# Kernel optimization log

Measured on AMD Instinct MI355X. Metric: run time of the kernel, lower is better.

Reference implementation:

```python
import jax, jax.numpy as jnp
import numpy as np

B, N, D, K, L, H, DFF = 2048, 64, 256, 32, 2, 8, 1024
TEMP = 10.0
EPS = 1e-10


def _ln(x, g, b):
    m = jnp.mean(x, -1, keepdims=True)
    v = jnp.mean((x - m) ** 2, -1, keepdims=True)
    return (x - m) * jax.lax.rsqrt(v + 1e-5) * g + b


def _mha(x, Wqkv, bqkv, Wo, bo):
    b, n, d = x.shape
    dh = d // H
    qkv = x @ Wqkv.T + bqkv                      # [b,n,3d]
    q, k, v = jnp.split(qkv, 3, axis=-1)
    q = q.reshape(b, n, H, dh)
    k = k.reshape(b, n, H, dh)
    v = v.reshape(b, n, H, dh)
    att = jnp.einsum('bqhd,bkhd->bhqk', q, k) / np.float32(np.sqrt(dh))
    att = jax.nn.softmax(att, axis=-1)
    o = jnp.einsum('bhqk,bkhd->bqhd', att, v).reshape(b, n, d)
    return o @ Wo.T + bo


def _encoder(x, Wqkv, bqkv, Wo, bo, ln1_g, ln1_b, ln2_g, ln2_b, W1, b1, W2, b2):
    # torch TransformerEncoder, norm_first=False (post-LN), dropout=0
    for l in range(L):
        x = _ln(x + _mha(x, Wqkv[l], bqkv[l], Wo[l], bo[l]), ln1_g[l], ln1_b[l])
        h = jax.nn.relu(x @ W1[l].T + b1[l]) @ W2[l].T + b2[l]
        x = _ln(x + h, ln2_g[l], ln2_b[l])
    return x


def _cluster_probs_from_emb(emb, mus):
    # ||x - tanh(mu)||^2 via expansion to avoid the [B,N,K,D] intermediate
    mt = jnp.tanh(mus)                                       # [K,D]
    d2 = (jnp.sum(emb ** 2, -1)[..., None]
          - 2.0 * jnp.einsum('bnd,kd->bnk', emb, mt)
          + jnp.sum(mt ** 2, -1))                            # [B,N,K]
    e = jnp.exp(-d2 / TEMP)
    return e / jnp.sum(e, -1, keepdims=True)


def _forward(input_series, init_logits, transition_logits,
             Wqkv, bqkv, Wo, bo, ln1_g, ln1_b, ln2_g, ln2_b,
             W1, b1, W2, b2, mus):
    prob_pi = jax.nn.softmax(init_logits, axis=0)            # [K]
    prob_A = jax.nn.softmax(transition_logits, axis=1)       # [K,K]
    emb_all = _encoder(input_series, Wqkv, bqkv, Wo, bo,
                       ln1_g, ln1_b, ln2_g, ln2_b, W1, b1, W2, b2)
    logits_all = _cluster_probs_from_emb(emb_all, mus)       # [B,N,K]

    log_emit = jnp.log(logits_all + EPS)                     # [B,N,K]
    lt0 = jax.nn.softmax(jnp.log(prob_pi + EPS)[None, :] + log_emit[:, 0], axis=1)

    def step(lt, le):
        lt = jax.nn.softmax(jnp.log(lt @ prob_A + EPS) + le, axis=1)
        return lt, lt

    _, rest = jax.lax.scan(step, lt0, jnp.swapaxes(log_emit[:, 1:], 0, 1))
    cluster_probs = jnp.concatenate([lt0[:, None], jnp.swapaxes(rest, 0, 1)], axis=1)
    entropy_loss = -jnp.mean(jnp.sum(cluster_probs * jnp.log(cluster_probs + EPS), -1))
    return cluster_probs, emb_all, prob_pi, prob_A, entropy_loss


def setup_inputs() -> dict:
    key = jax.random.key(0)
    ks = jax.random.split(key, 10)
    s = jnp.float32(0.02)
    return {
        'input_series': jax.random.normal(ks[0], (B, N, D), jnp.float32),
        'init_logits': jax.random.normal(ks[1], (K,), jnp.float32),
        'transition_logits': jax.random.normal(ks[2], (K, K), jnp.float32),
        'Wqkv': jax.random.normal(ks[3], (L, 3 * D, D), jnp.float32) * s,
        'bqkv': jnp.zeros((L, 3 * D), jnp.float32),
        'Wo': jax.random.normal(ks[4], (L, D, D), jnp.float32) * s,
        'bo': jnp.zeros((L, D), jnp.float32),
        'ln1_g': jnp.ones((L, D), jnp.float32),
        'ln1_b': jnp.zeros((L, D), jnp.float32),
        'ln2_g': jnp.ones((L, D), jnp.float32),
        'ln2_b': jnp.zeros((L, D), jnp.float32),
        'W1': jax.random.normal(ks[5], (L, DFF, D), jnp.float32) * s,
        'b1': jnp.zeros((L, DFF), jnp.float32),
        'W2': jax.random.normal(ks[6], (L, D, DFF), jnp.float32) * s,
        'b2': jnp.zeros((L, D), jnp.float32),
        'mus': jax.random.normal(ks[7], (K, D), jnp.float32),
    }


def reference(input_series, init_logits, transition_logits, Wqkv, bqkv, Wo, bo,
              ln1_g, ln1_b, ln2_g, ln2_b, W1, b1, W2, b2, mus):
    return _forward(input_series, init_logits, transition_logits, Wqkv, bqkv,
                    Wo, bo, ln1_g, ln1_b, ln2_g, ln2_b, W1, b1, W2, b2, mus)
```

## Files before the change

kernel.cpp:

```cpp
#include <hip/hip_runtime.h>

#define BB   2048
#define NNX  64
#define DD   256
#define KKC  32
#define LLN  2
#define HHN  8
#define DHH  32
#define DFFN 1024
#define BNT  (BB*NNX)

typedef short s16x8 __attribute__((ext_vector_type(8)));
typedef float f32x4 __attribute__((ext_vector_type(4)));

#define GLOAD_LDS16(gp, lp) __builtin_amdgcn_global_load_lds( \
    (const __attribute__((address_space(1))) void*)(gp),      \
    (__attribute__((address_space(3))) void*)(lp), 16, 0, 0)

#define WAITVM4() asm volatile("s_waitcnt vmcnt(4)" ::: "memory")
#define WAITVM0() asm volatile("s_waitcnt vmcnt(0)" ::: "memory")
#define WAITLGKM0() do { asm volatile("s_waitcnt lgkmcnt(0)" ::: "memory"); \
                         __builtin_amdgcn_sched_barrier(0); } while (0)
#define SBAR() __builtin_amdgcn_s_barrier()

__device__ __forceinline__ unsigned short f2bf(float f) {
  unsigned int u = __float_as_uint(f);
  u += 0x7fffu + ((u >> 16) & 1u);
  return (unsigned short)(u >> 16);
}
__device__ __forceinline__ float bf2f(unsigned short u) {
  return __uint_as_float(((unsigned int)u) << 16);
}

__global__ __launch_bounds__(256) void cvt_kernel(const float4* __restrict__ src,
                                                  ushort4* __restrict__ dst, int n4) {
  int i = blockIdx.x * 256 + threadIdx.x;
  int st = gridDim.x * 256;
  for (; i < n4; i += st) {
    float4 v = src[i];
    ushort4 o;
    o.x = f2bf(v.x); o.y = f2bf(v.y); o.z = f2bf(v.z); o.w = f2bf(v.w);
    dst[i] = o;
  }
}

__global__ __launch_bounds__(256) void cvtw_kernel(const float4* __restrict__ wq, ushort4* __restrict__ dq,
                                                   const float4* __restrict__ wo, ushort4* __restrict__ dov,
                                                   const float4* __restrict__ w1, ushort4* __restrict__ d1,
                                                   const float4* __restrict__ w2, ushort4* __restrict__ d2) {
  const int n0 = 98304, n1 = 32768, n2 = 131072, n3 = 131072;
  int i = blockIdx.x * 256 + threadIdx.x;
  int st = gridDim.x * 256;
  for (; i < n0 + n1 + n2 + n3; i += st) {
    const float4* s; ushort4* d; int j = i;
    if (j < n0) { s = wq; d = dq; }
    else if ((j -= n0) < n1) { s = wo; d = dov; }
    else if ((j -= n1) < n2) { s = w1; d = d1; }
    else { j -= n2; s = w2; d = d2; }
    float4 v = s[j];
    ushort4 o;
    o.x = f2bf(v.x); o.y = f2bf(v.y); o.z = f2bf(v.z); o.w = f2bf(v.w);
    d[j] = o;
  }
}

__global__ void mt_kernel(const float* __restrict__ mus, unsigned short* __restrict__ mtb,
                          float* __restrict__ mtn) {
  int k = threadIdx.x;
  if (k < 32) {
    float acc = 0.f;
    for (int d = 0; d < 256; d++) {
      float t = tanhf(mus[k * 256 + d]);
      mtb[k * 264 + d] = f2bf(t);
      acc += t * t;
    }
    mtn[k] = acc;
  }
}

__global__ void piA_kernel(const float* __restrict__ il, const float* __restrict__ tl,
                           float* __restrict__ d_pi, float* __restrict__ d_A,
                           float* __restrict__ d_ent) {
  int lane = threadIdx.x;
  if (lane == 0) *d_ent = 0.f;
  if (lane < 32) {
    float v = il[lane];
    float mx = v;
    #pragma unroll
    for (int off = 16; off; off >>= 1) mx = fmaxf(mx, __shfl_xor(mx, off, 32));
    float e = expf(v - mx), sm = e;
    #pragma unroll
    for (int off = 16; off; off >>= 1) sm += __shfl_xor(sm, off, 32);
    d_pi[lane] = e / sm;
    for (int r = 0; r < 32; r++) {
      float a = tl[r * 32 + lane];
      float m2 = a;
      #pragma unroll
      for (int off = 16; off; off >>= 1) m2 = fmaxf(m2, __shfl_xor(m2, off, 32));
      float e2 = expf(a - m2), s2 = e2;
      #pragma unroll
      for (int off = 16; off; off >>= 1) s2 += __shfl_xor(s2, off, 32);
      d_A[r * 32 + lane] = e2 / s2;
    }
  }
}

template <int EPI>
__global__ __launch_bounds__(256, 4) void gemm_nt(const unsigned short* __restrict__ A,
                                                  const unsigned short* __restrict__ Bw,
                                                  const float* __restrict__ bias,
                                                  unsigned short* __restrict__ outp,
                                                  int N, int K, int nx) {
  __shared__ unsigned short lds[16384];
  const int t = threadIdx.x;
  const int bid = blockIdx.x, nwg = gridDim.x;
  const int wg = (bid & 7) * (nwg >> 3) + (bid >> 3);
  const int m0 = (wg / nx) << 7;
  const int n0 = (wg % nx) << 7;
  const int lane = t & 63, w = t >> 6;
  const int wm = w >> 1, wn = w & 1;
  const int lr = lane & 15, lk = lane >> 4;

  const int r0 = t >> 2, sg = t & 3;
  const int s0 = sg ^ ((r0 >> 1) & 3);
  const int r1 = r0 + 64;
  const int s1 = sg ^ ((r1 >> 1) & 3);
  const int aoff0 = (m0 + r0) * K + s0 * 8;
  const int aoff1 = (m0 + r1) * K + s1 * 8;
  const int boff0 = (n0 + r0) * K + s0 * 8;
  const int boff1 = (n0 + r1) * K + s1 * 8;

#define STAGE(buf, k0) do {                                    \
    char* la = (char*)lds + (buf) * 16384;                     \
    GLOAD_LDS16(A + aoff0 + (k0), la + t * 16);                \
    GLOAD_LDS16(A + aoff1 + (k0), la + 4096 + t * 16);         \
    GLOAD_LDS16(Bw + boff0 + (k0), la + 8192 + t * 16);        \
    GLOAD_LDS16(Bw + boff1 + (k0), la + 12288 + t * 16);       \
  } while (0)

  f32x4 acc[4][4];
  #pragma unroll
  for (int i = 0; i < 4; i++)
    #pragma unroll
    for (int j = 0; j < 4; j++) acc[i][j] = (f32x4)(0.f);

  const int ra = wm * 64 + lr, rb = wn * 64 + lr;
  const int sla = lk ^ ((ra >> 1) & 3), slb = lk ^ ((rb >> 1) & 3);

  const int NT = K >> 5;
  STAGE(0, 0);
  STAGE(1, 32);
  WAITVM4();
  SBAR();

  int c = 0;
  for (int kt = 0; kt < NT; kt++) {
    s16x8 af[4], bf[4];
    {
      const unsigned short* ua = lds + c * 8192;
      const unsigned short* ub = ua + 4096;
      #pragma unroll
      for (int mf = 0; mf < 4; mf++)
        af[mf] = *(const s16x8*)&ua[(ra + mf * 16) * 32 + sla * 8];
      #pragma unroll
      for (int nf = 0; nf < 4; nf++)
        bf[nf] = *(const s16x8*)&ub[(rb + nf * 16) * 32 + slb * 8];
    }
    __builtin_amdgcn_s_setprio(1);
    #pragma unroll
    for (int mf = 0; mf < 4; mf++)
      #pragma unroll
      for (int nf = 0; nf < 4; nf++)
        acc[mf][nf] = __builtin_amdgcn_mfma_f32_16x16x32_bf16(af[mf], bf[nf], acc[mf][nf], 0, 0, 0);
    __builtin_amdgcn_s_setprio(0);
    SBAR();
    if (kt < NT - 2) {
      STAGE(c, (kt + 2) << 5);
      WAITVM4();
    } else if (kt == NT - 2) {
      WAITVM0();
    }
    SBAR();
    c ^= 1;
  }
#undef STAGE

  #pragma unroll
  for (int nf = 0; nf < 4; nf++) {
    int col = n0 + wn * 64 + nf * 16 + lr;
    float bv = bias[col];
    #pragma unroll
    for (int mf = 0; mf < 4; mf++)
      #pragma unroll
      for (int r = 0; r < 4; r++) {
        int row = m0 + wm * 64 + mf * 16 + lk * 4 + r;
        float v = acc[mf][nf][r] + bv;
        if (EPI == 1) v = fmaxf(v, 0.f);
        outp[(size_t)row * N + col] = f2bf(v);
      }
  }
}

template <bool WR32>
__global__ __launch_bounds__(512) void gemm_ln(const unsigned short* __restrict__ A,
                                               const unsigned short* __restrict__ Bw,
                                               const float* __restrict__ bias,
                                               const unsigned short* __restrict__ res,
                                               const float* __restrict__ g,
                                               const float* __restrict__ bta,
                                               unsigned short* __restrict__ xb,
                                               float* __restrict__ x32,
                                               int K) {
  __shared__ unsigned short As[128 * 64];
  __shared__ unsigned short Bs[256 * 64];
  __shared__ float stats[2][128][4];
  const int t = threadIdx.x;
  const int nwg = gridDim.x;
  const int bid = blockIdx.x;
  const int wg = (bid & 7) * (nwg >> 3) + (bid >> 3);
  const int m0 = wg << 7;

  const int lane = t & 63, w = t >> 6;
  const int wm = w >> 2, wn = w & 3;
  const int lr = lane & 15, lk = lane >> 4;

  size_t aoff[2], boff[4];
  #pragma unroll
  for (int p = 0; p < 2; p++) {
    int u = p * 512 + t;
    int row = u >> 3, sp = u & 7;
    int seg = sp ^ (((row >> 2) & 1) << 1);
    aoff[p] = (size_t)(m0 + row) * K + seg * 8;
  }
  #pragma unroll
  for (int p = 0; p < 4; p++) {
    int u = p * 512 + t;
    int row = u >> 3, sp = u & 7;
    int seg = sp ^ (((row >> 2) & 1) << 1);
    boff[p] = (size_t)row * K + seg * 8;
  }

  f32x4 acc[4][4];
  #pragma unroll
  for (int i = 0; i < 4; i++)
    #pragma unroll
    for (int j = 0; j < 4; j++) acc[i][j] = (f32x4)(0.f);

  for (int k0 = 0; k0 < K; k0 += 64) {
    #pragma unroll
    for (int p = 0; p < 2; p++)
      GLOAD_LDS16(A + aoff[p] + k0, (char*)As + (p * 512 + t) * 16);
    #pragma unroll
    for (int p = 0; p < 4; p++)
      GLOAD_LDS16(Bw + boff[p] + k0, (char*)Bs + (p * 512 + t) * 16);
    __syncthreads();
    #pragma unroll
    for (int z = 0; z < 2; z++) {
      s16x8 af[4], bfr[4];
      #pragma unroll
      for (int mf = 0; mf < 4; mf++) {
        int row = wm * 64 + mf * 16 + lr;
        int cc = (z * 4 + lk) ^ (((row >> 2) & 1) << 1);
        af[mf] = *(const s16x8*)&As[row * 64 + cc * 8];
      }
      #pragma unroll
      for (int nf = 0; nf < 4; nf++) {
        int row = wn * 64 + nf * 16 + lr;
        int cc = (z * 4 + lk) ^ (((row >> 2) & 1) << 1);
        bfr[nf] = *(const s16x8*)&Bs[row * 64 + cc * 8];
      }
      #pragma unroll
      for (int mf = 0; mf < 4; mf++)
        #pragma unroll
        for (int nf = 0; nf < 4; nf++)
          acc[mf][nf] = __builtin_amdgcn_mfma_f32_16x16x32_bf16(af[mf], bfr[nf], acc[mf][nf], 0, 0, 0);
    }
    __syncthreads();
  }

  float bv[4];
  #pragma unroll
  for (int nf = 0; nf < 4; nf++) bv[nf] = bias[wn * 64 + nf * 16 + lr];

  #pragma unroll
  for (int mf = 0; mf < 4; mf++) {
    #pragma unroll
    for (int r = 0; r < 4; r++) {
      int grow = m0 + wm * 64 + mf * 16 + lk * 4 + r;
      float s = 0.f, q = 0.f;
      #pragma unroll
      for (int nf = 0; nf < 4; nf++) {
        int col = wn * 64 + nf * 16 + lr;
        float v = acc[mf][nf][r] + bv[nf] + bf2f(res[(size_t)grow * 256 + col]);
        acc[mf][nf][r] = v;
        s += v; q += v * v;
      }
      #pragma unroll
      for (int off = 1; off < 16; off <<= 1) { s += __shfl_xor(s, off); q += __shfl_xor(q, off); }
      if (lr == 0) {
        int lrow = wm * 64 + mf * 16 + lk * 4 + r;
        stats[0][lrow][wn] = s;
        stats[1][lrow][wn] = q;
      }
    }
  }
  __syncthreads();

  float gv[4], bbv[4];
  #pragma unroll
  for (int nf = 0; nf < 4; nf++) {
    int col = wn * 64 + nf * 16 + lr;
    gv[nf] = g[col]; bbv[nf] = bta[col];
  }
  #pragma unroll
  for (int mf = 0; mf < 4; mf++) {
    #pragma unroll
    for (int r = 0; r < 4; r++) {
      int lrow = wm * 64 + mf * 16 + lk * 4 + r;
      int grow = m0 + lrow;
      float s4 = stats[0][lrow][0] + stats[0][lrow][1] + stats[0][lrow][2] + stats[0][lrow][3];
      float q4 = stats[1][lrow][0] + stats[1][lrow][1] + stats[1][lrow][2] + stats[1][lrow][3];
      float mean = s4 * (1.f / 256.f);
      float var = q4 * (1.f / 256.f) - mean * mean;
      float rs = rsqrtf(var + 1e-5f);
      #pragma unroll
      for (int nf = 0; nf < 4; nf++) {
        int col = wn * 64 + nf * 16 + lr;
        float val = (acc[mf][nf][r] - mean) * rs * gv[nf] + bbv[nf];
        xb[(size_t)grow * 256 + col] = f2bf(val);
        if (WR32) x32[(size_t)grow * 256 + col] = val;
      }
    }
  }
}

__global__ __launch_bounds__(64) void attn_kernel(const unsigned short* __restrict__ qkv,
                                                  unsigned short* __restrict__ ob) {
  __shared__ unsigned short al[6784];
  unsigned short* qs = al;
  unsigned short* ks = al + 2048;
  unsigned short* vs = al + 4608;
  unsigned short* vt = al;
  unsigned short* ps = al + 2176;
  const int bh = blockIdx.x;
  const int b = bh >> 3, h = bh & 7;
  const int lane = threadIdx.x;
  const int lr = lane & 15, lk = lane >> 4;

  #pragma unroll
  for (int p = 0; p < 4; p++) {
    int u = lane + p * 64;
    int row = u >> 2, seg = u & 3;
    size_t gb = (size_t)(b * 64 + row) * 768 + h * 32 + seg * 8;
    GLOAD_LDS16(qkv + gb, (char*)al + u * 16);
    GLOAD_LDS16(qkv + gb + 256, (char*)al + 4096 + u * 16);
    GLOAD_LDS16(qkv + gb + 512, (char*)al + 9216 + u * 16);
  }
  __syncthreads();

  s16x8 aq[4], bk[4], vchunk[4];
  #pragma unroll
  for (int mi = 0; mi < 4; mi++) aq[mi] = *(const s16x8*)&qs[(mi * 16 + lr) * 32 + lk * 8];
  #pragma unroll
  for (int nj = 0; nj < 4; nj++) bk[nj] = *(const s16x8*)&ks[(nj * 16 + lr) * 32 + lk * 8];
  const int vrow = lane >> 2, vcs = (lane & 3) * 8;
  #pragma unroll
  for (int q = 0; q < 4; q++)
    vchunk[q] = *(const s16x8*)&vs[(q * 16 + vrow) * 32 + vcs];
  WAITLGKM0();

  #pragma unroll
  for (int q = 0; q < 4; q++)
    #pragma unroll
    for (int j = 0; j < 8; j++)
      vt[(vcs + j) * 68 + q * 16 + vrow] = (unsigned short)vchunk[q][j];

  f32x4 s[4][4];
  #pragma unroll
  for (int i = 0; i < 4; i++)
    #pragma unroll
    for (int j = 0; j < 4; j++) s[i][j] = (f32x4)(0.f);
  #pragma unroll
  for (int mi = 0; mi < 4; mi++)
    #pragma unroll
    for (int nj = 0; nj < 4; nj++)
      s[mi][nj] = __builtin_amdgcn_mfma_f32_16x16x32_bf16(aq[mi], bk[nj], s[mi][nj], 0, 0, 0);

  const float scale = 0.17677669529663687f;
  #pragma unroll
  for (int mi = 0; mi < 4; mi++) {
    #pragma unroll
    for (int r = 0; r < 4; r++) {
      float t0 = s[mi][0][r] * scale, t1 = s[mi][1][r] * scale;
      float t2 = s[mi][2][r] * scale, t3 = s[mi][3][r] * scale;
      float mx = fmaxf(fmaxf(t0, t1), fmaxf(t2, t3));
      #pragma unroll
      for (int off = 8; off; off >>= 1) mx = fmaxf(mx, __shfl_xor(mx, off, 16));
      float e0 = expf(t0 - mx), e1 = expf(t1 - mx), e2 = expf(t2 - mx), e3 = expf(t3 - mx);
      float sm = e0 + e1 + e2 + e3;
      #pragma unroll
      for (int off = 8; off; off >>= 1) sm += __shfl_xor(sm, off, 16);
      float inv = 1.f / sm;
      int prow = mi * 16 + lk * 4 + r;
      ps[prow * 72 + lr + 0]  = f2bf(e0 * inv);
      ps[prow * 72 + lr + 16] = f2bf(e1 * inv);
      ps[prow * 72 + lr + 32] = f2bf(e2 * inv);
      ps[prow * 72 + lr + 48] = f2bf(e3 * inv);
    }
  }
  WAITLGKM0();

  f32x4 oacc[4][2];
  #pragma unroll
  for (int i = 0; i < 4; i++) { oacc[i][0] = (f32x4)(0.f); oacc[i][1] = (f32x4)(0.f); }
  #pragma unroll
  for (int kk = 0; kk < 2; kk++) {
    s16x8 bv[2];
    #pragma unroll
    for (int nf = 0; nf < 2; nf++)
      bv[nf] = *(const s16x8*)&vt[(nf * 16 + lr) * 68 + kk * 32 + lk * 8];
    #pragma unroll
    for (int mi = 0; mi < 4; mi++) {
      s16x8 ap = *(const s16x8*)&ps[(mi * 16 + lr) * 72 + kk * 32 + lk * 8];
      #pragma unroll
      for (int nf = 0; nf < 2; nf++)
        oacc[mi][nf] = __builtin_amdgcn_mfma_f32_16x16x32_bf16(ap, bv[nf], oacc[mi][nf], 0, 0, 0);
    }
  }
  #pragma unroll
  for (int mi = 0; mi < 4; mi++)
    #pragma unroll
    for (int nf = 0; nf < 2; nf++)
      #pragma unroll
      for (int r = 0; r < 4; r++) {
        int tok = mi * 16 + lk * 4 + r;
        int c = nf * 16 + lr;
        ob[(size_t)(b * 64 + tok) * 256 + h * 32 + c] = f2bf(oacc[mi][nf][r]);
      }
}

__global__ __launch_bounds__(256) void cluster_kernel(const unsigned short* __restrict__ xb,
                                                      const unsigned short* __restrict__ mtb,
                                                      const float* __restrict__ mtn,
                                                      float* __restrict__ log_emit) {
  __shared__ unsigned short ms[32 * 264];
  const int t = threadIdx.x;
  for (int i = t; i < 2112; i += 256)
    ((uint2*)ms)[i] = ((const uint2*)mtb)[i];
  const int lane = t & 63, w = t >> 6;
  const int lr = lane & 15, lk = lane >> 4;
  const float mtn0 = mtn[lr], mtn1 = mtn[16 + lr];
  __syncthreads();

  const size_t tok0 = (size_t)blockIdx.x * 256 + (size_t)w * 64;
  f32x4 s[4][2];
  #pragma unroll
  for (int i = 0; i < 4; i++) { s[i][0] = (f32x4)(0.f); s[i][1] = (f32x4)(0.f); }

  #pragma unroll
  for (int kk = 0; kk < 8; kk++) {
    s16x8 bf0 = *(const s16x8*)&ms[lr * 264 + lk * 8 + kk * 32];
    s16x8 bf1 = *(const s16x8*)&ms[(16 + lr) * 264 + lk * 8 + kk * 32];
    #pragma unroll
    for (int mi = 0; mi < 4; mi++) {
      s16x8 af = *(const s16x8*)&xb[(tok0 + mi * 16 + lr) * 256 + lk * 8 + kk * 32];
      s[mi][0] = __builtin_amdgcn_mfma_f32_16x16x32_bf16(af, bf0, s[mi][0], 0, 0, 0);
      s[mi][1] = __builtin_amdgcn_mfma_f32_16x16x32_bf16(af, bf1, s[mi][1], 0, 0, 0);
    }
  }

  #pragma unroll
  for (int mi = 0; mi < 4; mi++) {
    #pragma unroll
    for (int r = 0; r < 4; r++) {
      float l0 = (2.f * s[mi][0][r] - mtn0) * 0.1f;
      float l1 = (2.f * s[mi][1][r] - mtn1) * 0.1f;
      float mx = fmaxf(l0, l1);
      #pragma unroll
      for (int off = 8; off; off >>= 1) mx = fmaxf(mx, __shfl_xor(mx, off, 16));
      float e0 = expf(l0 - mx), e1 = expf(l1 - mx);
      float sm = e0 + e1;
      #pragma unroll
      for (int off = 8; off; off >>= 1) sm += __shfl_xor(sm, off, 16);
      float inv = 1.f / sm;
      size_t row = tok0 + mi * 16 + lk * 4 + r;
      log_emit[row * 32 + lr]      = logf(e0 * inv + 1e-10f);
      log_emit[row * 32 + 16 + lr] = logf(e1 * inv + 1e-10f);
    }
  }
}

__global__ __launch_bounds__(256) void scan_kernel(const float* __restrict__ log_emit,
                                                   const float* __restrict__ pi,
                                                   const float* __restrict__ A,
                                                   float* __restrict__ cp,
                                                   float* __restrict__ ent) {
  const int g = threadIdx.x >> 5, j = threadIdx.x & 31;
  const int batch = blockIdx.x * 8 + g;
  float regA[32];
  #pragma unroll
  for (int i = 0; i < 32; i++) regA[i] = A[i * 32 + j];
  const float* le = log_emit + (size_t)batch * 64 * 32;
  float* cpo = cp + (size_t)batch * 64 * 32;

  float u = logf(pi[j] + 1e-10f) + le[j];
  float mx = u;
  #pragma unroll
  for (int off = 16; off; off >>= 1) mx = fmaxf(mx, __shfl_xor(mx, off, 32));
  float e = expf(u - mx), sm = e;
  #pragma unroll
  for (int off = 16; off; off >>= 1) sm += __shfl_xor(sm, off, 32);
  float p = e / sm;
  cpo[j] = p;
  float enta = p * logf(p + 1e-10f);

  for (int n = 1; n < 64; n++) {
    float tt = 0.f;
    #pragma unroll
    for (int i = 0; i < 32; i++) tt += __shfl(p, i, 32) * regA[i];
    u = logf(tt + 1e-10f) + le[n * 32 + j];
    mx = u;
    #pragma unroll
    for (int off = 16; off; off >>= 1) mx = fmaxf(mx, __shfl_xor(mx, off, 32));
    e = expf(u - mx); sm = e;
    #pragma unroll
    for (int off = 16; off; off >>= 1) sm += __shfl_xor(sm, off, 32);
    p = e / sm;
    cpo[n * 32 + j] = p;
    enta += p * logf(p + 1e-10f);
  }
  #pragma unroll
  for (int off = 16; off; off >>= 1) enta += __shfl_xor(enta, off, 32);
  if (j == 0) atomicAdd(ent, -enta * (1.f / (2048.f * 64.f)));
}

extern "C" void kernel_launch(void* const* d_in, const int* in_sizes, int n_in,
                              void* d_out, int out_size, void* d_ws, size_t ws_size,
                              hipStream_t stream) {
  const float* input = (const float*)d_in[0];
  const float* init_logits = (const float*)d_in[1];
  const float* trans = (const float*)d_in[2];
  const float* Wqkv = (const float*)d_in[3];
  const float* bqkv = (const float*)d_in[4];
  const float* Wo = (const float*)d_in[5];
  const float* bo = (const float*)d_in[6];
  const float* ln1g = (const float*)d_in[7];
  const float* ln1b = (const float*)d_in[8];
  const float* ln2g = (const float*)d_in[9];
  const float* ln2b = (const float*)d_in[10];
  const float* W1 = (const float*)d_in[11];
  const float* b1 = (const float*)d_in[12];
  const float* W2 = (const float*)d_in[13];
  const float* b2 = (const float*)d_in[14];
  const float* mus = (const float*)d_in[15];

  float* out = (float*)d_out;
  float* cp = out;
  float* x = out + 4194304;
  float* d_pi = out + 37748736;
  float* d_A = out + 37748768;
  float* d_ent = out + 37749792;

  char* ws = (char*)d_ws;
  unsigned short* qkv = (unsigned short*)ws;
  unsigned short* hb = (unsigned short*)ws;
  float* log_emit = (float*)ws;
  unsigned short* ob = (unsigned short*)(ws + 268435456ull);
  unsigned short* xb = (unsigned short*)(ws + 335544320ull);
  unsigned short* wq_b = (unsigned short*)(ws + 402653184ull);
  unsigned short* wo_b = (unsigned short*)(ws + 402653184ull + 786432ull);
  unsigned short* w1_b = (unsigned short*)(ws + 402653184ull + 1048576ull);
  unsigned short* w2_b = (unsigned short*)(ws + 402653184ull + 2097152ull);
  unsigned short* mtb = (unsigned short*)(ws + 402653184ull + 3145728ull);
  float* mtn = (float*)(ws + 402653184ull + 3178496ull);

  cvt_kernel<<<2048, 256, 0, stream>>>((const float4*)input, (ushort4*)xb, BNT * 256 / 4);
  cvtw_kernel<<<512, 256, 0, stream>>>((const float4*)Wqkv, (ushort4*)wq_b,
                                       (const float4*)Wo, (ushort4*)wo_b,
                                       (const float4*)W1, (ushort4*)w1_b,
                                       (const float4*)W2, (ushort4*)w2_b);
  mt_kernel<<<1, 64, 0, stream>>>(mus, mtb, mtn);
  piA_kernel<<<1, 64, 0, stream>>>(init_logits, trans, d_pi, d_A, d_ent);

  for (int l = 0; l < 2; l++) {
    gemm_nt<0><<<6144, 256, 0, stream>>>(xb, wq_b + l * 196608, bqkv + l * 768,
                                         qkv, 768, 256, 6);
    attn_kernel<<<16384, 64, 0, stream>>>(qkv, ob);
    gemm_ln<false><<<1024, 512, 0, stream>>>(ob, wo_b + l * 65536, bo + l * 256,
                                             xb, ln1g + l * 256, ln1b + l * 256,
                                             xb, nullptr, 256);
    gemm_nt<1><<<8192, 256, 0, stream>>>(xb, w1_b + l * 262144, b1 + l * 1024,
                                         hb, 1024, 256, 8);
    if (l == LLN - 1)
      gemm_ln<true><<<1024, 512, 0, stream>>>(hb, w2_b + l * 262144, b2 + l * 256,
                                              xb, ln2g + l * 256, ln2b + l * 256,
                                              xb, x, 1024);
    else
      gemm_ln<false><<<1024, 512, 0, stream>>>(hb, w2_b + l * 262144, b2 + l * 256,
                                               xb, ln2g + l * 256, ln2b + l * 256,
                                               xb, nullptr, 1024);
  }

  cluster_kernel<<<512, 256, 0, stream>>>(xb, mtb, mtn, log_emit);
  scan_kernel<<<256, 256, 0, stream>>>(log_emit, d_pi, d_A, cp, d_ent);
}
```

Before: 1.141 ms.

## Split FFN2 GEMM+LayerNorm into tiled gemm_nt with residual plus separate LN kernel

Replaces the fused gemm_ln kernel for the second FFN projection (K=1024) with the generic 128x128-tile gemm_nt, extended with a residual-add epilogue that writes a bf16 pre-norm buffer, followed by a standalone per-token LayerNorm kernel. The goal is to use the better-pipelined gemm_nt main loop (double-buffered global_load_lds) for the long-K GEMM instead of the 128x256 full-row tile that gemm_ln needs for fused LN, which runs with fewer blocks. In exchange it adds an extra round trip through HBM for the intermediate activations and rounds the pre-LN sum to bf16.

```diff
diff --git a/kernel.cpp b/kernel.cpp
--- a/kernel.cpp
+++ b/kernel.cpp
@@ -109,6 +109,7 @@
 __global__ __launch_bounds__(256, 4) void gemm_nt(const unsigned short* __restrict__ A,
                                                   const unsigned short* __restrict__ Bw,
                                                   const float* __restrict__ bias,
+                                                  const unsigned short* __restrict__ res,
                                                   unsigned short* __restrict__ outp,
                                                   int N, int K, int nx) {
   __shared__ unsigned short lds[16384];
@@ -194,9 +195,11 @@
       #pragma unroll
       for (int r = 0; r < 4; r++) {
         int row = m0 + wm * 64 + mf * 16 + lk * 4 + r;
+        size_t o = (size_t)row * N + col;
         float v = acc[mf][nf][r] + bv;
         if (EPI == 1) v = fmaxf(v, 0.f);
-        outp[(size_t)row * N + col] = f2bf(v);
+        if (EPI == 2) v += bf2f(res[o]);
+        outp[o] = f2bf(v);
       }
   }
 }
@@ -331,6 +334,36 @@
         if (WR32) x32[(size_t)grow * 256 + col] = val;
       }
     }
+  }
+}
+
+template <bool WR32>
+__global__ __launch_bounds__(256) void ln_kernel(const unsigned short* __restrict__ yin,
+                                                 const float* __restrict__ g,
+                                                 const float* __restrict__ bta,
+                                                 unsigned short* __restrict__ xb,
+                                                 float* __restrict__ xout) {
+  const int w = threadIdx.x >> 6, lane = threadIdx.x & 63;
+  const size_t tok = (size_t)blockIdx.x * 4 + w;
+  ushort4 u = *((const ushort4*)(yin + tok * 256) + lane);
+  float v[4] = {bf2f(u.x), bf2f(u.y), bf2f(u.z), bf2f(u.w)};
+  float s = v[0] + v[1] + v[2] + v[3];
+  float q = v[0] * v[0] + v[1] * v[1] + v[2] * v[2] + v[3] * v[3];
+  #pragma unroll
+  for (int off = 1; off < 64; off <<= 1) { s += __shfl_xor(s, off); q += __shfl_xor(q, off); }
+  float mean = s * (1.f / 256.f);
+  float var = q * (1.f / 256.f) - mean * mean;
+  float rs = rsqrtf(var + 1e-5f);
+  int d0 = lane * 4;
+  float o0 = (v[0] - mean) * rs * g[d0 + 0] + bta[d0 + 0];
+  float o1 = (v[1] - mean) * rs * g[d0 + 1] + bta[d0 + 1];
+  float o2 = (v[2] - mean) * rs * g[d0 + 2] + bta[d0 + 2];
+  float o3 = (v[3] - mean) * rs * g[d0 + 3] + bta[d0 + 3];
+  ushort4 ub = {f2bf(o0), f2bf(o1), f2bf(o2), f2bf(o3)};
+  *((ushort4*)(xb + tok * 256) + lane) = ub;
+  if (WR32) {
+    float4 fo = {o0, o1, o2, o3};
+    *((float4*)(xout + tok * 256) + lane) = fo;
   }
 }
 
@@ -566,6 +599,7 @@
   unsigned short* hb = (unsigned short*)ws;
   float* log_emit = (float*)ws;
   unsigned short* ob = (unsigned short*)(ws + 268435456ull);
+  unsigned short* y2 = ob;
   unsigned short* xb = (unsigned short*)(ws + 335544320ull);
   unsigned short* wq_b = (unsigned short*)(ws + 402653184ull);
   unsigned short* wo_b = (unsigned short*)(ws + 402653184ull + 786432ull);
@@ -584,21 +618,19 @@
 
   for (int l = 0; l < 2; l++) {
     gemm_nt<0><<<6144, 256, 0, stream>>>(xb, wq_b + l * 196608, bqkv + l * 768,
-                                         qkv, 768, 256, 6);
+                                         nullptr, qkv, 768, 256, 6);
     attn_kernel<<<16384, 64, 0, stream>>>(qkv, ob);
     gemm_ln<false><<<1024, 512, 0, stream>>>(ob, wo_b + l * 65536, bo + l * 256,
                                              xb, ln1g + l * 256, ln1b + l * 256,
                                              xb, nullptr, 256);
     gemm_nt<1><<<8192, 256, 0, stream>>>(xb, w1_b + l * 262144, b1 + l * 1024,
-                                         hb, 1024, 256, 8);
+                                         nullptr, hb, 1024, 256, 8);
+    gemm_nt<2><<<2048, 256, 0, stream>>>(hb, w2_b + l * 262144, b2 + l * 256,
+                                         xb, y2, 256, 1024, 2);
     if (l == LLN - 1)
-      gemm_ln<true><<<1024, 512, 0, stream>>>(hb, w2_b + l * 262144, b2 + l * 256,
-                                              xb, ln2g + l * 256, ln2b + l * 256,
-                                              xb, x, 1024);
+      ln_kernel<true><<<32768, 256, 0, stream>>>(y2, ln2g + l * 256, ln2b + l * 256, xb, x);
     else
-      gemm_ln<false><<<1024, 512, 0, stream>>>(hb, w2_b + l * 262144, b2 + l * 256,
-                                               xb, ln2g + l * 256, ln2b + l * 256,
-                                               xb, nullptr, 1024);
+      ln_kernel<false><<<32768, 256, 0, stream>>>(y2, ln2g + l * 256, ln2b + l * 256, xb, nullptr);
   }
 
   cluster_kernel<<<512, 256, 0, stream>>>(xb, mtb, mtn, log_emit);
```

Result: slower. 1.290 ms (+13.0%).

## Quantize FFN hidden activations and W2 to FP8 and run second FFN GEMM in FP8

Applied to the files above, without the earlier changes.

The FFN1 epilogue now writes the ReLU output as scaled FP8 (e4m3) instead of bf16, and W2 is converted to scaled FP8. A new gemm_ln_fp8 kernel uses FP8 MFMA with the residual-add and LayerNorm fused in, undoing the scales in the epilogue. This halves the traffic for the large hidden tensor and doubles MFMA throughput for the W2 GEMM. It costs accuracy through FP8 rounding and fixed scale factors, and the new kernel uses a simple unpipelined single-buffer loop.

```diff
diff --git a/kernel.cpp b/kernel.cpp
--- a/kernel.cpp
+++ b/kernel.cpp
@@ -32,6 +32,24 @@
   return __uint_as_float(((unsigned int)u) << 16);
 }
 
+__device__ __forceinline__ unsigned char f2fp8(float f) {
+  unsigned u = __float_as_uint(f);
+  unsigned lsb = (u >> 20) & 1u;
+  u += 0x7FFFFu + lsb;
+  int e = (int)((u >> 23) & 255u) - 120;
+  if (e <= 0) {
+    int q = (int)(f * 512.f + 0.5f);
+    return (unsigned char)q;
+  }
+  if (e > 15) return 0x7E;
+  return (unsigned char)((e << 3) | ((u >> 20) & 7u));
+}
+__device__ __forceinline__ unsigned char f2fp8s(float f) {
+  unsigned s = __float_as_uint(f) >> 31;
+  float a = fminf(fabsf(f), 448.f);
+  return (unsigned char)((s << 7) | f2fp8(a));
+}
+
 __global__ __launch_bounds__(256) void cvt_kernel(const float4* __restrict__ src,
                                                   ushort4* __restrict__ dst, int n4) {
   int i = blockIdx.x * 256 + threadIdx.x;
@@ -47,20 +65,27 @@
 __global__ __launch_bounds__(256) void cvtw_kernel(const float4* __restrict__ wq, ushort4* __restrict__ dq,
                                                    const float4* __restrict__ wo, ushort4* __restrict__ dov,
                                                    const float4* __restrict__ w1, ushort4* __restrict__ d1,
-                                                   const float4* __restrict__ w2, ushort4* __restrict__ d2) {
+                                                   const float4* __restrict__ w2, uchar4* __restrict__ d2) {
   const int n0 = 98304, n1 = 32768, n2 = 131072, n3 = 131072;
   int i = blockIdx.x * 256 + threadIdx.x;
   int st = gridDim.x * 256;
   for (; i < n0 + n1 + n2 + n3; i += st) {
-    const float4* s; ushort4* d; int j = i;
-    if (j < n0) { s = wq; d = dq; }
-    else if ((j -= n0) < n1) { s = wo; d = dov; }
-    else if ((j -= n1) < n2) { s = w1; d = d1; }
-    else { j -= n2; s = w2; d = d2; }
-    float4 v = s[j];
-    ushort4 o;
-    o.x = f2bf(v.x); o.y = f2bf(v.y); o.z = f2bf(v.z); o.w = f2bf(v.w);
-    d[j] = o;
+    int j = i;
+    if (j < n0) {
+      float4 v = wq[j];
+      dq[j] = (ushort4){f2bf(v.x), f2bf(v.y), f2bf(v.z), f2bf(v.w)};
+    } else if ((j -= n0) < n1) {
+      float4 v = wo[j];
+      dov[j] = (ushort4){f2bf(v.x), f2bf(v.y), f2bf(v.z), f2bf(v.w)};
+    } else if ((j -= n1) < n2) {
+      float4 v = w1[j];
+      d1[j] = (ushort4){f2bf(v.x), f2bf(v.y), f2bf(v.z), f2bf(v.w)};
+    } else {
+      j -= n2;
+      float4 v = w2[j];
+      d2[j] = (uchar4){f2fp8s(v.x * 64.f), f2fp8s(v.y * 64.f),
+                       f2fp8s(v.z * 64.f), f2fp8s(v.w * 64.f)};
+    }
   }
 }
 
@@ -109,7 +134,7 @@
 __global__ __launch_bounds__(256, 4) void gemm_nt(const unsigned short* __restrict__ A,
                                                   const unsigned short* __restrict__ Bw,
                                                   const float* __restrict__ bias,
-                                                  unsigned short* __restrict__ outp,
+                                                  void* __restrict__ outp,
                                                   int N, int K, int nx) {
   __shared__ unsigned short lds[16384];
   const int t = threadIdx.x;
@@ -194,9 +219,14 @@
       #pragma unroll
       for (int r = 0; r < 4; r++) {
         int row = m0 + wm * 64 + mf * 16 + lk * 4 + r;
+        size_t o = (size_t)row * N + col;
         float v = acc[mf][nf][r] + bv;
-        if (EPI == 1) v = fmaxf(v, 0.f);
-        outp[(size_t)row * N + col] = f2bf(v);
+        if (EPI == 0) {
+          ((unsigned short*)outp)[o] = f2bf(v);
+        } else {
+          float h = fminf(fmaxf(v, 0.f) * 8.f, 448.f);
+          ((unsigned char*)outp)[o] = f2fp8(h);
+        }
       }
   }
 }
@@ -320,6 +350,125 @@
       int grow = m0 + lrow;
       float s4 = stats[0][lrow][0] + stats[0][lrow][1] + stats[0][lrow][2] + stats[0][lrow][3];
       float q4 = stats[1][lrow][0] + stats[1][lrow][1] + stats[1][lrow][2] + stats[1][lrow][3];
+      float mean = s4 * (1.f / 256.f);
+      float var = q4 * (1.f / 256.f) - mean * mean;
+      float rs = rsqrtf(var + 1e-5f);
+      #pragma unroll
+      for (int nf = 0; nf < 4; nf++) {
+        int col = wn * 64 + nf * 16 + lr;
+        float val = (acc[mf][nf][r] - mean) * rs * gv[nf] + bbv[nf];
+        xb[(size_t)grow * 256 + col] = f2bf(val);
+        if (WR32) x32[(size_t)grow * 256 + col] = val;
+      }
+    }
+  }
+}
+
+template <bool WR32>
+__global__ __launch_bounds__(512) void gemm_ln_fp8(const unsigned char* __restrict__ A,
+                                                   const unsigned char* __restrict__ Bw,
+                                                   const float* __restrict__ bias,
+                                                   const unsigned short* __restrict__ res,
+                                                   const float* __restrict__ g,
+                                                   const float* __restrict__ bta,
+                                                   unsigned short* __restrict__ xb,
+                                                   float* __restrict__ x32,
+                                                   int K) {
+  __shared__ unsigned char lds8[24576];
+  float* stats = (float*)lds8;
+  const int t = threadIdx.x;
+  const int nwg = gridDim.x;
+  const int bid = blockIdx.x;
+  const int wg = (bid & 7) * (nwg >> 3) + (bid >> 3);
+  const int m0 = wg << 7;
+
+  const int lane = t & 63, w = t >> 6;
+  const int wm = w >> 2, wn = w & 3;
+  const int lr = lane & 15, lk = lane >> 4;
+
+  const int auu = t >> 8, arow = (t >> 1) & 127, asg = t & 1;
+  const size_t aoff = (size_t)(m0 + arow) * K + auu * 32 + asg * 16;
+  size_t boff[2];
+  #pragma unroll
+  for (int p = 0; p < 2; p++) {
+    int idx = p * 512 + t;
+    int buu = idx >> 9, brow = (idx >> 1) & 255, bsg = idx & 1;
+    boff[p] = (size_t)brow * K + buu * 32 + bsg * 16;
+  }
+
+  f32x4 acc[4][4];
+  #pragma unroll
+  for (int i = 0; i < 4; i++)
+    #pragma unroll
+    for (int j = 0; j < 4; j++) acc[i][j] = (f32x4)(0.f);
+
+  for (int k0 = 0; k0 < K; k0 += 64) {
+    GLOAD_LDS16(A + aoff + k0, (char*)lds8 + t * 16);
+    GLOAD_LDS16(Bw + boff[0] + k0, (char*)lds8 + 8192 + t * 16);
+    GLOAD_LDS16(Bw + boff[1] + k0, (char*)lds8 + 16384 + t * 16);
+    __syncthreads();
+    #pragma unroll
+    for (int kk = 0; kk < 2; kk++) {
+      long long af[4], bf[4];
+      #pragma unroll
+      for (int mf = 0; mf < 4; mf++)
+        af[mf] = *(const long long*)&lds8[kk * 4096 + (wm * 64 + mf * 16 + lr) * 32 + lk * 8];
+      #pragma unroll
+      for (int nf = 0; nf < 4; nf++)
+        bf[nf] = *(const long long*)&lds8[8192 + kk * 8192 + (wn * 64 + nf * 16 + lr) * 32 + lk * 8];
+      #pragma unroll
+      for (int mf = 0; mf < 4; mf++)
+        #pragma unroll
+        for (int nf = 0; nf < 4; nf++)
+          acc[mf][nf] = __builtin_amdgcn_mfma_f32_16x16x32_fp8_fp8(af[mf], bf[nf], acc[mf][nf], 0, 0, 0);
+    }
+    __syncthreads();
+  }
+
+  const float isc = 1.f / 512.f;
+  float bv[4];
+  #pragma unroll
+  for (int nf = 0; nf < 4; nf++) bv[nf] = bias[wn * 64 + nf * 16 + lr];
+
+  #pragma unroll
+  for (int mf = 0; mf < 4; mf++) {
+    #pragma unroll
+    for (int r = 0; r < 4; r++) {
+      int grow = m0 + wm * 64 + mf * 16 + lk * 4 + r;
+      float s = 0.f, q = 0.f;
+      #pragma unroll
+      for (int nf = 0; nf < 4; nf++) {
+        int col = wn * 64 + nf * 16 + lr;
+        float v = acc[mf][nf][r] * isc + bv[nf] + bf2f(res[(size_t)grow * 256 + col]);
+        acc[mf][nf][r] = v;
+        s += v; q += v * v;
+      }
+      #pragma unroll
+      for (int off = 1; off < 16; off <<= 1) { s += __shfl_xor(s, off); q += __shfl_xor(q, off); }
+      if (lr == 0) {
+        int lrow = wm * 64 + mf * 16 + lk * 4 + r;
+        stats[lrow * 4 + wn] = s;
+        stats[512 + lrow * 4 + wn] = q;
+      }
+    }
+  }
+  __syncthreads();
+
+  float gv[4], bbv[4];
+  #pragma unroll
+  for (int nf = 0; nf < 4; nf++) {
+    int col = wn * 64 + nf * 16 + lr;
+    gv[nf] = g[col]; bbv[nf] = bta[col];
+  }
+  #pragma unroll
+  for (int mf = 0; mf < 4; mf++) {
+    #pragma unroll
+    for (int r = 0; r < 4; r++) {
+      int lrow = wm * 64 + mf * 16 + lk * 4 + r;
+      int grow = m0 + lrow;
+      float s4 = stats[lrow * 4 + 0] + stats[lrow * 4 + 1] + stats[lrow * 4 + 2] + stats[lrow * 4 + 3];
+      float q4 = stats[512 + lrow * 4 + 0] + stats[512 + lrow * 4 + 1]
+               + stats[512 + lrow * 4 + 2] + stats[512 + lrow * 4 + 3];
       float mean = s4 * (1.f / 256.f);
       float var = q4 * (1.f / 256.f) - mean * mean;
       float rs = rsqrtf(var + 1e-5f);
@@ -563,14 +712,14 @@
 
   char* ws = (char*)d_ws;
   unsigned short* qkv = (unsigned short*)ws;
-  unsigned short* hb = (unsigned short*)ws;
+  unsigned char* hb = (unsigned char*)ws;
   float* log_emit = (float*)ws;
   unsigned short* ob = (unsigned short*)(ws + 268435456ull);
   unsigned short* xb = (unsigned short*)(ws + 335544320ull);
   unsigned short* wq_b = (unsigned short*)(ws + 402653184ull);
   unsigned short* wo_b = (unsigned short*)(ws + 402653184ull + 786432ull);
   unsigned short* w1_b = (unsigned short*)(ws + 402653184ull + 1048576ull);
-  unsigned short* w2_b = (unsigned short*)(ws + 402653184ull + 2097152ull);
+  unsigned char* w2_f = (unsigned char*)(ws + 402653184ull + 2097152ull);
   unsigned short* mtb = (unsigned short*)(ws + 402653184ull + 3145728ull);
   float* mtn = (float*)(ws + 402653184ull + 3178496ull);
 
@@ -578,7 +727,7 @@
   cvtw_kernel<<<512, 256, 0, stream>>>((const float4*)Wqkv, (ushort4*)wq_b,
                                        (const float4*)Wo, (ushort4*)wo_b,
                                        (const float4*)W1, (ushort4*)w1_b,
-                                       (const float4*)W2, (ushort4*)w2_b);
+                                       (const float4*)W2, (uchar4*)w2_f);
   mt_kernel<<<1, 64, 0, stream>>>(mus, mtb, mtn);
   piA_kernel<<<1, 64, 0, stream>>>(init_logits, trans, d_pi, d_A, d_ent);
 
@@ -592,13 +741,13 @@
     gemm_nt<1><<<8192, 256, 0, stream>>>(xb, w1_b + l * 262144, b1 + l * 1024,
                                          hb, 1024, 256, 8);
     if (l == LLN - 1)
-      gemm_ln<true><<<1024, 512, 0, stream>>>(hb, w2_b + l * 262144, b2 + l * 256,
-                                              xb, ln2g + l * 256, ln2b + l * 256,
-                                              xb, x, 1024);
+      gemm_ln_fp8<true><<<1024, 512, 0, stream>>>(hb, w2_f + l * 262144, b2 + l * 256,
+                                                  xb, ln2g + l * 256, ln2b + l * 256,
+                                                  xb, x, 1024);
     else
-      gemm_ln<false><<<1024, 512, 0, stream>>>(hb, w2_b + l * 262144, b2 + l * 256,
-                                               xb, ln2g + l * 256, ln2b + l * 256,
-                                               xb, nullptr, 1024);
+      gemm_ln_fp8<false><<<1024, 512, 0, stream>>>(hb, w2_f + l * 262144, b2 + l * 256,
+                                                   xb, ln2g + l * 256, ln2b + l * 256,
+                                                   xb, nullptr, 1024);
   }
 
   cluster_kernel<<<512, 256, 0, stream>>>(xb, mtb, mtn, log_emit);
```

Measured after the change: 1.111 ms. -2.7%, faster.

## Run out-projection and FFN-down GEMMs in FP8 with scaled operands

Applied to the files above, without the earlier changes.

Converts Wo and W2 weights to scaled FP8 (e4m3-style), has attention output and the FFN ReLU activations written as scaled FP8, and rewrites the LayerNorm-fused GEMM to use 16x16x32 fp8 MFMA with a dequant scale in the epilogue. This halves the bytes moved for the hidden activation buffer and attention output and doubles MFMA throughput for those GEMMs. It also merges the two tiny setup kernels into one launch. It risks accuracy loss from 8-bit quantization with hand-picked fixed scales.

```diff
diff --git a/kernel.cpp b/kernel.cpp
--- a/kernel.cpp
+++ b/kernel.cpp
@@ -32,6 +32,24 @@
   return __uint_as_float(((unsigned int)u) << 16);
 }
 
+__device__ __forceinline__ unsigned char f2fp8(float f) {
+  unsigned u = __float_as_uint(f);
+  unsigned lsb = (u >> 20) & 1u;
+  u += 0x7FFFFu + lsb;
+  int e = (int)((u >> 23) & 255u) - 120;
+  if (e <= 0) {
+    int q = (int)(f * 512.f + 0.5f);
+    return (unsigned char)q;
+  }
+  if (e > 15) return 0x7E;
+  return (unsigned char)((e << 3) | ((u >> 20) & 7u));
+}
+__device__ __forceinline__ unsigned char f2fp8s(float f) {
+  unsigned s = __float_as_uint(f) >> 31;
+  float a = fminf(fabsf(f), 448.f);
+  return (unsigned char)((s << 7) | f2fp8(a));
+}
+
 __global__ __launch_bounds__(256) void cvt_kernel(const float4* __restrict__ src,
                                                   ushort4* __restrict__ dst, int n4) {
   int i = blockIdx.x * 256 + threadIdx.x;
@@ -45,62 +63,70 @@
 }
 
 __global__ __launch_bounds__(256) void cvtw_kernel(const float4* __restrict__ wq, ushort4* __restrict__ dq,
-                                                   const float4* __restrict__ wo, ushort4* __restrict__ dov,
+                                                   const float4* __restrict__ wo, uchar4* __restrict__ dov,
                                                    const float4* __restrict__ w1, ushort4* __restrict__ d1,
-                                                   const float4* __restrict__ w2, ushort4* __restrict__ d2) {
+                                                   const float4* __restrict__ w2, uchar4* __restrict__ d2) {
   const int n0 = 98304, n1 = 32768, n2 = 131072, n3 = 131072;
   int i = blockIdx.x * 256 + threadIdx.x;
   int st = gridDim.x * 256;
   for (; i < n0 + n1 + n2 + n3; i += st) {
-    const float4* s; ushort4* d; int j = i;
-    if (j < n0) { s = wq; d = dq; }
-    else if ((j -= n0) < n1) { s = wo; d = dov; }
-    else if ((j -= n1) < n2) { s = w1; d = d1; }
-    else { j -= n2; s = w2; d = d2; }
-    float4 v = s[j];
-    ushort4 o;
-    o.x = f2bf(v.x); o.y = f2bf(v.y); o.z = f2bf(v.z); o.w = f2bf(v.w);
-    d[j] = o;
-  }
-}
-
-__global__ void mt_kernel(const float* __restrict__ mus, unsigned short* __restrict__ mtb,
-                          float* __restrict__ mtn) {
-  int k = threadIdx.x;
-  if (k < 32) {
-    float acc = 0.f;
-    for (int d = 0; d < 256; d++) {
-      float t = tanhf(mus[k * 256 + d]);
-      mtb[k * 264 + d] = f2bf(t);
-      acc += t * t;
-    }
-    mtn[k] = acc;
-  }
-}
-
-__global__ void piA_kernel(const float* __restrict__ il, const float* __restrict__ tl,
-                           float* __restrict__ d_pi, float* __restrict__ d_A,
-                           float* __restrict__ d_ent) {
+    int j = i;
+    if (j < n0) {
+      float4 v = wq[j];
+      dq[j] = (ushort4){f2bf(v.x), f2bf(v.y), f2bf(v.z), f2bf(v.w)};
+    } else if ((j -= n0) < n1) {
+      float4 v = wo[j];
+      dov[j] = (uchar4){f2fp8s(v.x * 64.f), f2fp8s(v.y * 64.f),
+                        f2fp8s(v.z * 64.f), f2fp8s(v.w * 64.f)};
+    } else if ((j -= n1) < n2) {
+      float4 v = w1[j];
+      d1[j] = (ushort4){f2bf(v.x), f2bf(v.y), f2bf(v.z), f2bf(v.w)};
+    } else {
+      j -= n2;
+      float4 v = w2[j];
+      d2[j] = (uchar4){f2fp8s(v.x * 64.f), f2fp8s(v.y * 64.f),
+                       f2fp8s(v.z * 64.f), f2fp8s(v.w * 64.f)};
+    }
+  }
+}
+
+__global__ void mtpi_kernel(const float* __restrict__ mus, unsigned short* __restrict__ mtb,
+                            float* __restrict__ mtn,
+                            const float* __restrict__ il, const float* __restrict__ tl,
+                            float* __restrict__ d_pi, float* __restrict__ d_A,
+                            float* __restrict__ d_ent) {
   int lane = threadIdx.x;
-  if (lane == 0) *d_ent = 0.f;
-  if (lane < 32) {
-    float v = il[lane];
-    float mx = v;
-    #pragma unroll
-    for (int off = 16; off; off >>= 1) mx = fmaxf(mx, __shfl_xor(mx, off, 32));
-    float e = expf(v - mx), sm = e;
-    #pragma unroll
-    for (int off = 16; off; off >>= 1) sm += __shfl_xor(sm, off, 32);
-    d_pi[lane] = e / sm;
-    for (int r = 0; r < 32; r++) {
-      float a = tl[r * 32 + lane];
-      float m2 = a;
-      #pragma unroll
-      for (int off = 16; off; off >>= 1) m2 = fmaxf(m2, __shfl_xor(m2, off, 32));
-      float e2 = expf(a - m2), s2 = e2;
-      #pragma unroll
-      for (int off = 16; off; off >>= 1) s2 += __shfl_xor(s2, off, 32);
-      d_A[r * 32 + lane] = e2 / s2;
+  if (blockIdx.x == 0) {
+    if (lane < 32) {
+      float acc = 0.f;
+      for (int d = 0; d < 256; d++) {
+        float t = tanhf(mus[lane * 256 + d]);
+        mtb[lane * 264 + d] = f2bf(t);
+        acc += t * t;
+      }
+      mtn[lane] = acc;
+    }
+  } else {
+    if (lane == 0) *d_ent = 0.f;
+    if (lane < 32) {
+      float v = il[lane];
+      float mx = v;
+      #pragma unroll
+      for (int off = 16; off; off >>= 1) mx = fmaxf(mx, __shfl_xor(mx, off, 32));
+      float e = expf(v - mx), sm = e;
+      #pragma unroll
+      for (int off = 16; off; off >>= 1) sm += __shfl_xor(sm, off, 32);
+      d_pi[lane] = e / sm;
+      for (int r = 0; r < 32; r++) {
+        float a = tl[r * 32 + lane];
+        float m2 = a;
+        #pragma unroll
+        for (int off = 16; off; off >>= 1) m2 = fmaxf(m2, __shfl_xor(m2, off, 32));
+        float e2 = expf(a - m2), s2 = e2;
+        #pragma unroll
+        for (int off = 16; off; off >>= 1) s2 += __shfl_xor(s2, off, 32);
+        d_A[r * 32 + lane] = e2 / s2;
+      }
     }
   }
 }
@@ -109,7 +135,7 @@
 __global__ __launch_bounds__(256, 4) void gemm_nt(const unsigned short* __restrict__ A,
                                                   const unsigned short* __restrict__ Bw,
                                                   const float* __restrict__ bias,
-                                                  unsigned short* __restrict__ outp,
+                                                  void* __restrict__ outp,
                                                   int N, int K, int nx) {
   __shared__ unsigned short lds[16384];
   const int t = threadIdx.x;
@@ -194,26 +220,30 @@
       #pragma unroll
       for (int r = 0; r < 4; r++) {
         int row = m0 + wm * 64 + mf * 16 + lk * 4 + r;
+        size_t o = (size_t)row * N + col;
         float v = acc[mf][nf][r] + bv;
-        if (EPI == 1) v = fmaxf(v, 0.f);
-        outp[(size_t)row * N + col] = f2bf(v);
+        if (EPI == 0) {
+          ((unsigned short*)outp)[o] = f2bf(v);
+        } else {
+          float h = fminf(fmaxf(v, 0.f) * 8.f, 448.f);
+          ((unsigned char*)outp)[o] = f2fp8(h);
+        }
       }
   }
 }
 
 template <bool WR32>
-__global__ __launch_bounds__(512) void gemm_ln(const unsigned short* __restrict__ A,
-                                               const unsigned short* __restrict__ Bw,
-                                               const float* __restrict__ bias,
-                                               const unsigned short* __restrict__ res,
-                                               const float* __restrict__ g,
-                                               const float* __restrict__ bta,
-                                               unsigned short* __restrict__ xb,
-                                               float* __restrict__ x32,
-                                               int K) {
-  __shared__ unsigned short As[128 * 64];
-  __shared__ unsigned short Bs[256 * 64];
-  __shared__ float stats[2][128][4];
+__global__ __launch_bounds__(512) void gemm_ln_fp8(const unsigned char* __restrict__ A,
+                                                   const unsigned char* __restrict__ Bw,
+                                                   const float* __restrict__ bias,
+                                                   const unsigned short* __restrict__ res,
+                                                   const float* __restrict__ g,
+                                                   const float* __restrict__ bta,
+                                                   unsigned short* __restrict__ xb,
+                                                   float* __restrict__ x32,
+                                                   int K, float isc) {
+  __shared__ unsigned char lds8[24576];
+  float* stats = (float*)lds8;
   const int t = threadIdx.x;
   const int nwg = gridDim.x;
   const int bid = blockIdx.x;
@@ -224,20 +254,14 @@
   const int wm = w >> 2, wn = w & 3;
   const int lr = lane & 15, lk = lane >> 4;
 
-  size_t aoff[2], boff[4];
+  const int auu = t >> 8, arow = (t >> 1) & 127, asg = t & 1;
+  const size_t aoff = (size_t)(m0 + arow) * K + auu * 32 + asg * 16;
+  size_t boff[2];
   #pragma unroll
   for (int p = 0; p < 2; p++) {
-    int u = p * 512 + t;
-    int row = u >> 3, sp = u & 7;
-    int seg = sp ^ (((row >> 2) & 1) << 1);
-    aoff[p] = (size_t)(m0 + row) * K + seg * 8;
-  }
-  #pragma unroll
-  for (int p = 0; p < 4; p++) {
-    int u = p * 512 + t;
-    int row = u >> 3, sp = u & 7;
-    int seg = sp ^ (((row >> 2) & 1) << 1);
-    boff[p] = (size_t)row * K + seg * 8;
+    int idx = p * 512 + t;
+    int buu = idx >> 9, brow = (idx >> 1) & 255, bsg = idx & 1;
+    boff[p] = (size_t)brow * K + buu * 32 + bsg * 16;
   }
 
   f32x4 acc[4][4];
@@ -247,33 +271,24 @@
     for (int j = 0; j < 4; j++) acc[i][j] = (f32x4)(0.f);
 
   for (int k0 = 0; k0 < K; k0 += 64) {
-    #pragma unroll
-    for (int p = 0; p < 2; p++)
-      GLOAD_LDS16(A + aoff[p] + k0, (char*)As + (p * 512 + t) * 16);
-    #pragma unroll
-    for (int p = 0; p < 4; p++)
-      GLOAD_LDS16(Bw + boff[p] + k0, (char*)Bs + (p * 512 + t) * 16);
+    GLOAD_LDS16(A + aoff + k0, (char*)lds8 + t * 16);
+    GLOAD_LDS16(Bw + boff[0] + k0, (char*)lds8 + 8192 + t * 16);
+    GLOAD_LDS16(Bw + boff[1] + k0, (char*)lds8 + 16384 + t * 16);
     __syncthreads();
     #pragma unroll
-    for (int z = 0; z < 2; z++) {
-      s16x8 af[4], bfr[4];
-      #pragma unroll
-      for (int mf = 0; mf < 4; mf++) {
-        int row = wm * 64 + mf * 16 + lr;
-        int cc = (z * 4 + lk) ^ (((row >> 2) & 1) << 1);
-        af[mf] = *(const s16x8*)&As[row * 64 + cc * 8];
-      }
-      #pragma unroll
-      for (int nf = 0; nf < 4; nf++) {
-        int row = wn * 64 + nf * 16 + lr;
-        int cc = (z * 4 + lk) ^ (((row >> 2) & 1) << 1);
-        bfr[nf] = *(const s16x8*)&Bs[row * 64 + cc * 8];
-      }
+    for (int kk = 0; kk < 2; kk++) {
+      long long af[4], bf[4];
+      #pragma unroll
+      for (int mf = 0; mf < 4; mf++)
+        af[mf] = *(const long long*)&lds8[kk * 4096 + (wm * 64 + mf * 16 + lr) * 32 + lk * 8];
+      #pragma unroll
+      for (int nf = 0; nf < 4; nf++)
+        bf[nf] = *(const long long*)&lds8[8192 + kk * 8192 + (wn * 64 + nf * 16 + lr) * 32 + lk * 8];
       #pragma unroll
       for (int mf = 0; mf < 4; mf++)
         #pragma unroll
         for (int nf = 0; nf < 4; nf++)
-          acc[mf][nf] = __builtin_amdgcn_mfma_f32_16x16x32_bf16(af[mf], bfr[nf], acc[mf][nf], 0, 0, 0);
+          acc[mf][nf] = __builtin_amdgcn_mfma_f32_16x16x32_fp8_fp8(af[mf], bf[nf], acc[mf][nf], 0, 0, 0);
     }
     __syncthreads();
   }
@@ -291,7 +306,7 @@
       #pragma unroll
       for (int nf = 0; nf < 4; nf++) {
         int col = wn * 64 + nf * 16 + lr;
-        float v = acc[mf][nf][r] + bv[nf] + bf2f(res[(size_t)grow * 256 + col]);
+        float v = acc[mf][nf][r] * isc + bv[nf] + bf2f(res[(size_t)grow * 256 + col]);
         acc[mf][nf][r] = v;
         s += v; q += v * v;
       }
@@ -299,8 +314,8 @@
       for (int off = 1; off < 16; off <<= 1) { s += __shfl_xor(s, off); q += __shfl_xor(q, off); }
       if (lr == 0) {
         int lrow = wm * 64 + mf * 16 + lk * 4 + r;
-        stats[0][lrow][wn] = s;
-        stats[1][lrow][wn] = q;
+        stats[lrow * 4 + wn] = s;
+        stats[512 + lrow * 4 + wn] = q;
       }
     }
   }
@@ -318,8 +333,9 @@
     for (int r = 0; r < 4; r++) {
       int lrow = wm * 64 + mf * 16 + lk * 4 + r;
       int grow = m0 + lrow;
-      float s4 = stats[0][lrow][0] + stats[0][lrow][1] + stats[0][lrow][2] + stats[0][lrow][3];
-      float q4 = stats[1][lrow][0] + stats[1][lrow][1] + stats[1][lrow][2] + stats[1][lrow][3];
+      float s4 = stats[lrow * 4 + 0] + stats[lrow * 4 + 1] + stats[lrow * 4 + 2] + stats[lrow * 4 + 3];
+      float q4 = stats[512 + lrow * 4 + 0] + stats[512 + lrow * 4 + 1]
+               + stats[512 + lrow * 4 + 2] + stats[512 + lrow * 4 + 3];
       float mean = s4 * (1.f / 256.f);
       float var = q4 * (1.f / 256.f) - mean * mean;
       float rs = rsqrtf(var + 1e-5f);
@@ -335,7 +351,7 @@
 }
 
 __global__ __launch_bounds__(64) void attn_kernel(const unsigned short* __restrict__ qkv,
-                                                  unsigned short* __restrict__ ob) {
+                                                  unsigned char* __restrict__ ob) {
   __shared__ unsigned short al[6784];
   unsigned short* qs = al;
   unsigned short* ks = al + 2048;
@@ -435,7 +451,7 @@
       for (int r = 0; r < 4; r++) {
         int tok = mi * 16 + lk * 4 + r;
         int c = nf * 16 + lr;
-        ob[(size_t)(b * 64 + tok) * 256 + h * 32 + c] = f2bf(oacc[mi][nf][r]);
+        ob[(size_t)(b * 64 + tok) * 256 + h * 32 + c] = f2fp8s(oacc[mi][nf][r] * 16.f);
       }
 }
 
@@ -563,42 +579,41 @@
 
   char* ws = (char*)d_ws;
   unsigned short* qkv = (unsigned short*)ws;
-  unsigned short* hb = (unsigned short*)ws;
+  unsigned char* hb = (unsigned char*)ws;
   float* log_emit = (float*)ws;
-  unsigned short* ob = (unsigned short*)(ws + 268435456ull);
+  unsigned char* ob = (unsigned char*)(ws + 268435456ull);
   unsigned short* xb = (unsigned short*)(ws + 335544320ull);
   unsigned short* wq_b = (unsigned short*)(ws + 402653184ull);
-  unsigned short* wo_b = (unsigned short*)(ws + 402653184ull + 786432ull);
+  unsigned char* wo_f = (unsigned char*)(ws + 402653184ull + 786432ull);
   unsigned short* w1_b = (unsigned short*)(ws + 402653184ull + 1048576ull);
-  unsigned short* w2_b = (unsigned short*)(ws + 402653184ull + 2097152ull);
+  unsigned char* w2_f = (unsigned char*)(ws + 402653184ull + 2097152ull);
   unsigned short* mtb = (unsigned short*)(ws + 402653184ull + 3145728ull);
   float* mtn = (float*)(ws + 402653184ull + 3178496ull);
 
   cvt_kernel<<<2048, 256, 0, stream>>>((const float4*)input, (ushort4*)xb, BNT * 256 / 4);
   cvtw_kernel<<<512, 256, 0, stream>>>((const float4*)Wqkv, (ushort4*)wq_b,
-                                       (const float4*)Wo, (ushort4*)wo_b,
+                                       (const float4*)Wo, (uchar4*)wo_f,
                                        (const float4*)W1, (ushort4*)w1_b,
-                                       (const float4*)W2, (ushort4*)w2_b);
-  mt_kernel<<<1, 64, 0, stream>>>(mus, mtb, mtn);
-  piA_kernel<<<1, 64, 0, stream>>>(init_logits, trans, d_pi, d_A, d_ent);
+                                       (const float4*)W2, (uchar4*)w2_f);
+  mtpi_kernel<<<2, 64, 0, stream>>>(mus, mtb, mtn, init_logits, trans, d_pi, d_A, d_ent);
 
   for (int l = 0; l < 2; l++) {
     gemm_nt<0><<<6144, 256, 0, stream>>>(xb, wq_b + l * 196608, bqkv + l * 768,
                                          qkv, 768, 256, 6);
     attn_kernel<<<16384, 64, 0, stream>>>(qkv, ob);
-    gemm_ln<false><<<1024, 512, 0, stream>>>(ob, wo_b + l * 65536, bo + l * 256,
-                                             xb, ln1g + l * 256, ln1b + l * 256,
-                                             xb, nullptr, 256);
+    gemm_ln_fp8<false><<<1024, 512, 0, stream>>>(ob, wo_f + l * 65536, bo + l * 256,
+                                                 xb, ln1g + l * 256, ln1b + l * 256,
+                                                 xb, nullptr, 256, 1.f / 1024.f);
     gemm_nt<1><<<8192, 256, 0, stream>>>(xb, w1_b + l * 262144, b1 + l * 1024,
                                          hb, 1024, 256, 8);
     if (l == LLN - 1)
-      gemm_ln<true><<<1024, 512, 0, stream>>>(hb, w2_b + l * 262144, b2 + l * 256,
-                                              xb, ln2g + l * 256, ln2b + l * 256,
-                                              xb, x, 1024);
+      gemm_ln_fp8<true><<<1024, 512, 0, stream>>>(hb, w2_f + l * 262144, b2 + l * 256,
+                                                  xb, ln2g + l * 256, ln2b + l * 256,
+                                                  xb, x, 1024, 1.f / 512.f);
     else
-      gemm_ln<false><<<1024, 512, 0, stream>>>(hb, w2_b + l * 262144, b2 + l * 256,
-                                               xb, ln2g + l * 256, ln2b + l * 256,
-                                               xb, nullptr, 1024);
+      gemm_ln_fp8<false><<<1024, 512, 0, stream>>>(hb, w2_f + l * 262144, b2 + l * 256,
+                                                   xb, ln2g + l * 256, ln2b + l * 256,
+                                                   xb, nullptr, 1024, 1.f / 512.f);
   }
 
   cluster_kernel<<<512, 256, 0, stream>>>(xb, mtb, mtn, log_emit);
```

After: 1.127 ms. Within noise of the previous version (-1.3%).
